# Kernel optimization log

Hardware: AMD Instinct MI355X
Metric: run time of the kernel (lower is better)

Reference implementation:

```python
import jax, jax.numpy as jnp
import numpy as np

NUM_CLASSES = 80
STRIDES = (8, 16, 32)


def _decode(p, stride):
    # p: [B, 5+C, H, W] raw head -> [B, HW, 5+C] decoded (xy in px, wh=exp*stride)
    B, C, H, W = p.shape
    ys, xs = jnp.meshgrid(jnp.arange(H), jnp.arange(W), indexing='ij')
    grid = jnp.stack([xs, ys], -1).reshape(H * W, 2).astype(p.dtype)
    out = p.reshape(B, C, H * W).transpose(0, 2, 1)
    xy = (out[..., :2] + grid) * stride
    wh = jnp.exp(out[..., 2:4]) * stride
    out = jnp.concatenate([xy, wh, out[..., 4:]], -1)
    es = jnp.full((H * W,), float(stride), p.dtype)
    return out, grid[:, 0], grid[:, 1], es


def _pairwise_iou(gt, pr):
    # gt [G,4] cxcywh, pr [A,4] -> [G,A]
    gt_tl = gt[:, None, :2] - gt[:, None, 2:] * 0.5
    gt_br = gt[:, None, :2] + gt[:, None, 2:] * 0.5
    pr_tl = pr[None, :, :2] - pr[None, :, 2:] * 0.5
    pr_br = pr[None, :, :2] + pr[None, :, 2:] * 0.5
    tl = jnp.maximum(gt_tl, pr_tl)
    br = jnp.minimum(gt_br, pr_br)
    en = jnp.all(tl < br, -1).astype(gt.dtype)
    inter = jnp.prod(br - tl, -1) * en
    a_gt = jnp.prod(gt[:, 2:], -1)[:, None]
    a_pr = jnp.prod(pr[:, 2:], -1)[None, :]
    return inter / (a_gt + a_pr - inter + 1e-16)


def _assign(gt_boxes, gt_cls, bbox, clsp, objp, xg, yg, es):
    # SimOTA assignment for one image (all fixed-shape; non-candidate anchors
    # are masked out via huge cost instead of boolean gather).
    G = gt_boxes.shape[0]
    xc = (xg + 0.5) * es  # [A] anchor centers
    yc = (yg + 0.5) * es
    gl = gt_boxes[:, 0:1] - 0.5 * gt_boxes[:, 2:3]
    gr = gt_boxes[:, 0:1] + 0.5 * gt_boxes[:, 2:3]
    gt_ = gt_boxes[:, 1:2] - 0.5 * gt_boxes[:, 3:4]
    gb = gt_boxes[:, 1:2] + 0.5 * gt_boxes[:, 3:4]
    in_box = (xc[None] > gl) & (xc[None] < gr) & (yc[None] > gt_) & (yc[None] < gb)  # [G,A]
    r = 2.5 * es[None]
    in_ctr = ((xc[None] > gt_boxes[:, 0:1] - r) & (xc[None] < gt_boxes[:, 0:1] + r)
              & (yc[None] > gt_boxes[:, 1:2] - r) & (yc[None] < gt_boxes[:, 1:2] + r))
    fg_cand = jnp.any(in_box, 0) | jnp.any(in_ctr, 0)  # [A]
    in_both = in_box & in_ctr  # [G,A]

    ious = _pairwise_iou(gt_boxes, bbox)  # [G,A]
    ious_m = jnp.where(fg_cand[None, :], ious, 0.0)
    iou_cost = -jnp.log(ious_m + 1e-8)

    # pairwise cls BCE cost: bce(sqrt(sigmoid(cls)*sigmoid(obj)), onehot(gt)).sum(-1)
    p = jnp.sqrt(jax.nn.sigmoid(clsp) * jax.nn.sigmoid(objp[:, None]))  # [A,C]
    lp = jnp.maximum(jnp.log(p), -100.0)
    l1p = jnp.maximum(jnp.log1p(-p), -100.0)
    t = jax.nn.one_hot(gt_cls, NUM_CLASSES, dtype=p.dtype)  # [G,C]
    cls_cost = -(jnp.einsum('ac,gc->ga', lp - l1p, t) + jnp.sum(l1p, -1)[None, :])

    cost = (cls_cost + 3.0 * iou_cost
            + 1e5 * (~in_both).astype(p.dtype)
            + 1e9 * (~fg_cand)[None, :].astype(p.dtype))

    # dynamic-k: k_g = clamp(sum(top10 ious), min=1)
    topk_ious, _ = jax.lax.top_k(ious_m, 10)
    dyn_k = jnp.clip(topk_ious.sum(-1).astype(jnp.int32), 1, None)  # [G]
    rank = jnp.argsort(jnp.argsort(cost, axis=1), axis=1)  # rank of each anchor per gt
    matching = (rank < dyn_k[:, None]) & fg_cand[None, :]  # [G,A]
    # resolve anchors matched to multiple gts: keep min-cost gt
    multi = matching.sum(0) > 1
    best = jnp.argmin(cost, 0)
    matching = jnp.where(multi[None, :], jnp.arange(G)[:, None] == best[None, :], matching)

    fg = jnp.any(matching, 0)  # [A]
    matched_gt = jnp.argmax(matching, 0)  # [A]
    pred_iou = jnp.sum(matching * ious, 0)  # [A]
    matched_cls = gt_cls[matched_gt]
    return fg, matched_gt, pred_iou, matched_cls


def _giou_loss(b, g):
    tl = jnp.maximum(b[..., :2] - b[..., 2:] * 0.5, g[..., :2] - g[..., 2:] * 0.5)
    br = jnp.minimum(b[..., :2] + b[..., 2:] * 0.5, g[..., :2] + g[..., 2:] * 0.5)
    area_b = jnp.prod(b[..., 2:], -1)
    area_g = jnp.prod(g[..., 2:], -1)
    en = jnp.all(tl < br, -1).astype(b.dtype)
    inter = jnp.prod(br - tl, -1) * en
    union = area_b + area_g - inter
    iou = inter / (union + 1e-16)
    ctl = jnp.minimum(b[..., :2] - b[..., 2:] * 0.5, g[..., :2] - g[..., 2:] * 0.5)
    cbr = jnp.maximum(b[..., :2] + b[..., 2:] * 0.5, g[..., :2] + g[..., 2:] * 0.5)
    area_c = jnp.maximum(jnp.prod(cbr - ctl, -1), 1e-16)
    giou = iou - (area_c - union) / area_c
    return 1.0 - jnp.clip(giou, -1.0, 1.0)


def _bce_logits(x, t):
    return jnp.maximum(x, 0.0) - x * t + jnp.log1p(jnp.exp(-jnp.abs(x)))


def _forward(p8, p16, p32, labels):
    outs, xo, yo, eo = [], [], [], []
    for p, s in zip((p8, p16, p32), STRIDES):
        o, x, y, e = _decode(p, s)
        outs.append(o); xo.append(x); yo.append(y); eo.append(e)
    outputs = jnp.concatenate(outs, 1)  # [B, A, 5+C]
    xg = jnp.concatenate(xo); yg = jnp.concatenate(yo); es = jnp.concatenate(eo)

    bbox = outputs[..., :4]
    obj = outputs[..., 4]
    cls = outputs[..., 5:]
    gt_boxes = labels[..., :4]
    gt_cls = labels[..., 4].astype(jnp.int32)

    # assignment runs under no_grad in torch
    det = jax.lax.stop_gradient(outputs)
    fg, matched_gt, pred_iou, matched_cls = jax.vmap(
        lambda gb, gc, o: _assign(gb, gc, o[..., :4], o[..., 5:], o[..., 4], xg, yg, es)
    )(gt_boxes, gt_cls, det)

    fgf = fg.astype(outputs.dtype)  # [B,A]
    reg_t = jnp.take_along_axis(gt_boxes, matched_gt[..., None], axis=1)  # [B,A,4]
    cls_t = (jax.nn.one_hot(matched_cls, NUM_CLASSES, dtype=outputs.dtype)
             * pred_iou[..., None] * fgf[..., None])

    loss_iou = jnp.sum(_giou_loss(bbox, reg_t) * fgf)
    loss_obj = jnp.sum(_bce_logits(obj, fgf))
    loss_cls = jnp.sum(_bce_logits(cls, cls_t) * fgf[..., None])
    num_fg = jnp.maximum(jnp.sum(fgf), 1.0)
    return (5.0 * loss_iou + loss_obj + loss_cls) / num_fg


def setup_inputs() -> dict:
    key = jax.random.key(0)
    k1, k2, k3, k4, k5, k6 = jax.random.split(key, 6)
    B, NGT = 32, 20
    p8 = jax.random.normal(k1, (B, 5 + NUM_CLASSES, 80, 80), dtype=jnp.float32)
    p16 = jax.random.normal(k2, (B, 5 + NUM_CLASSES, 40, 40), dtype=jnp.float32)
    p32 = jax.random.normal(k3, (B, 5 + NUM_CLASSES, 20, 20), dtype=jnp.float32)
    cxy = jax.random.uniform(k4, (B, NGT, 2), dtype=jnp.float32, minval=32.0, maxval=608.0)
    wh = jax.random.uniform(k5, (B, NGT, 2), dtype=jnp.float32, minval=16.0, maxval=128.0)
    cls = jax.random.randint(k6, (B, NGT, 1), 0, NUM_CLASSES).astype(jnp.float32)
    labels = jnp.concatenate([cxy, wh, cls], -1)
    return {"p8": p8, "p16": p16, "p32": p32, "labels": labels}


def reference(p8, p16, p32, labels):
    return _forward(p8, p16, p32, labels)
```

## Files before the change

### kernel.cpp

```cpp
#include <hip/hip_runtime.h>
#include <cstdint>
#include <cstddef>

#define NA 8400
#define NAP 8448
#define NB 32
#define NG 20
#define NCL 80
#define NBLK 33

__device__ __forceinline__ float frcp(float x) { return __builtin_amdgcn_rcpf(x); }
__device__ __forceinline__ float bce0(float x) {
  return fmaxf(x, 0.0f) + __logf(1.0f + __expf(-fabsf(x)));
}

__device__ __forceinline__ void anchor_info(int a, const float* p8, const float* p16,
                                            const float* p32, int b, const float*& base,
                                            int& hw, int& HW, int& xg, int& yg, float& fs) {
  if (a < 6400)      { hw = a;        HW = 6400; xg = hw % 80; yg = hw / 80; fs = 8.f;
                       base = p8  + (size_t)b * 85 * 6400; }
  else if (a < 8000) { hw = a - 6400; HW = 1600; xg = hw % 40; yg = hw / 40; fs = 16.f;
                       base = p16 + (size_t)b * 85 * 1600; }
  else               { hw = a - 8000; HW = 400;  xg = hw % 20; yg = hw / 20; fs = 32.f;
                       base = p32 + (size_t)b * 85 * 400; }
}

__device__ __forceinline__ float iou_raw(float gx, float gy, float gw, float gh, float4 p) {
  float gtlx = gx - gw * 0.5f, gtly = gy - gh * 0.5f;
  float gbrx = gx + gw * 0.5f, gbry = gy + gh * 0.5f;
  float ptlx = p.x - p.z * 0.5f, ptly = p.y - p.w * 0.5f;
  float pbrx = p.x + p.z * 0.5f, pbry = p.y + p.w * 0.5f;
  float tlx = fmaxf(gtlx, ptlx), tly = fmaxf(gtly, ptly);
  float brx = fminf(gbrx, pbrx), bry = fminf(gbry, pbry);
  float inter = ((tlx < brx) && (tly < bry)) ? (brx - tlx) * (bry - tly) : 0.0f;
  float ag = gw * gh, ap = p.z * p.w;
  return inter * frcp(ag + ap - inter + 1e-16f);
}

__device__ __forceinline__ float giou_loss(float4 bb, float gx, float gy, float gw, float gh) {
  float btlx = bb.x - bb.z * 0.5f, btly = bb.y - bb.w * 0.5f;
  float bbrx = bb.x + bb.z * 0.5f, bbry = bb.y + bb.w * 0.5f;
  float gtlx = gx - gw * 0.5f, gtly = gy - gh * 0.5f;
  float gbrx = gx + gw * 0.5f, gbry = gy + gh * 0.5f;
  float tlx = fmaxf(btlx, gtlx), tly = fmaxf(btly, gtly);
  float brx = fminf(bbrx, gbrx), bry = fminf(bbry, gbry);
  float area_b = bb.z * bb.w, area_g = gw * gh;
  float inter = ((tlx < brx) && (tly < bry)) ? (brx - tlx) * (bry - tly) : 0.0f;
  float uni = area_b + area_g - inter;
  float iou = inter / (uni + 1e-16f);
  float ctlx = fminf(btlx, gtlx), ctly = fminf(btly, gtly);
  float cbrx = fmaxf(bbrx, gbrx), cbry = fmaxf(bbry, gbry);
  float area_c = fmaxf((cbrx - ctlx) * (cbry - ctly), 1e-16f);
  float giou = iou - (area_c - uni) / area_c;
  giou = fminf(fmaxf(giou, -1.0f), 1.0f);
  return 1.0f - giou;
}

__device__ __forceinline__ void block_argmin(float& v, int& i, volatile float* s_v,
                                             volatile int* s_i, int tid) {
#pragma unroll
  for (int off = 32; off; off >>= 1) {
    float ov = __shfl_down(v, off, 64);
    int   oi = __shfl_down(i, off, 64);
    if (ov < v || (ov == v && oi < i)) { v = ov; i = oi; }
  }
  if ((tid & 63) == 0) { s_v[tid >> 6] = v; s_i[tid >> 6] = i; }
  __syncthreads();
  v = s_v[0]; i = s_i[0];
#pragma unroll
  for (int w = 1; w < 4; ++w) {
    float ov = s_v[w]; int oi = s_i[w];
    if (ov < v || (ov == v && oi < i)) { v = ov; i = oi; }
  }
}

__global__ __launch_bounds__(256) void k1(const float* __restrict__ p8,
                                          const float* __restrict__ p16,
                                          const float* __restrict__ p32,
                                          const float* __restrict__ labels,
                                          int* __restrict__ n_fg_cnt,
                                          int* __restrict__ fg_list,
                                          unsigned int* __restrict__ am_c,
                                          float4* __restrict__ bbox_c,
                                          float* __restrict__ lso_c,
                                          unsigned int* __restrict__ match_c,
                                          float* __restrict__ blk_obj) {
  __shared__ float s_gt[NG * 4];
  __shared__ unsigned int s_wcnt[4];
  __shared__ float s_part[4];
  __shared__ unsigned int s_base;
  int blk = blockIdx.x, b = blockIdx.y, tid = threadIdx.x, lane = tid & 63, wid = tid >> 6;

  if (tid < NG) {
    s_gt[tid * 4 + 0] = labels[((size_t)b * NG + tid) * 5 + 0];
    s_gt[tid * 4 + 1] = labels[((size_t)b * NG + tid) * 5 + 1];
    s_gt[tid * 4 + 2] = labels[((size_t)b * NG + tid) * 5 + 2];
    s_gt[tid * 4 + 3] = labels[((size_t)b * NG + tid) * 5 + 3];
  }
  __syncthreads();

  int a = blk * 256 + tid;
  match_c[(size_t)b * NAP + a] = 0u;

  bool fg = false;
  unsigned int msk = 0u;
  float bce_obj = 0.0f, obj = 0.0f;
  const float* base = nullptr; int hw = 0, HW = 0, xg = 0, yg = 0; float fs = 8.f;
  if (a < NA) {
    anchor_info(a, p8, p16, p32, b, base, hw, HW, xg, yg, fs);
    obj = base[4 * HW + hw];
    bce_obj = bce0(obj);
    float xc = ((float)xg + 0.5f) * fs;
    float yc = ((float)yg + 0.5f) * fs;
    float r = 2.5f * fs;
#pragma unroll
    for (int g = 0; g < NG; ++g) {
      float gx = s_gt[g * 4 + 0], gy = s_gt[g * 4 + 1];
      float gw = s_gt[g * 4 + 2], gh = s_gt[g * 4 + 3];
      bool inb = (xc > gx - 0.5f * gw) && (xc < gx + 0.5f * gw) &&
                 (yc > gy - 0.5f * gh) && (yc < gy + 0.5f * gh);
      bool inc = (xc > gx - r) && (xc < gx + r) && (yc > gy - r) && (yc < gy + r);
      fg = fg || inb || inc;
      if (inb && inc) msk |= (1u << g);
    }
  }

  unsigned long long bm = __ballot(fg);
#pragma unroll
  for (int off = 32; off; off >>= 1) bce_obj += __shfl_down(bce_obj, off, 64);
  if (lane == 0) { s_wcnt[wid] = (unsigned int)__popcll(bm); s_part[wid] = bce_obj; }
  __syncthreads();
  if (tid == 0) {
    unsigned int cnt = s_wcnt[0] + s_wcnt[1] + s_wcnt[2] + s_wcnt[3];
    s_base = cnt ? (unsigned int)atomicAdd(&n_fg_cnt[b], (int)cnt) : 0u;
    blk_obj[b * NBLK + blk] = s_part[0] + s_part[1] + s_part[2] + s_part[3];
  }
  __syncthreads();

  if (!fg) return;
  unsigned int pos = s_base;
  for (int w = 0; w < wid; ++w) pos += s_wcnt[w];
  pos += (unsigned int)__popcll(bm & ((1ull << lane) - 1ull));
  size_t bo = (size_t)b * NAP;
  int ci = (int)pos;
  fg_list[bo + ci] = a;
  am_c[bo + ci] = msk;

  float v0 = base[hw];
  float v1 = base[HW + hw];
  float v2 = base[2 * HW + hw];
  float v3 = base[3 * HW + hw];
  bbox_c[bo + ci] = make_float4((v0 + (float)xg) * fs, (v1 + (float)yg) * fs,
                                __expf(v2) * fs, __expf(v3) * fs);
  float uo = __logf(1.0f + __expf(-fabsf(obj)));
  lso_c[bo + ci] = fminf(obj, 0.0f) - uo;
}

__global__ __launch_bounds__(256) void k23(const float* __restrict__ p8,
                                           const float* __restrict__ p16,
                                           const float* __restrict__ p32,
                                           const float* __restrict__ labels,
                                           const int* __restrict__ fg_list,
                                           const int* __restrict__ n_fg,
                                           const float* __restrict__ lso_c,
                                           const unsigned int* __restrict__ am_c,
                                           const float4* __restrict__ bbox_c,
                                           float* __restrict__ sb_c,
                                           float* __restrict__ cost_tbl,
                                           float* __restrict__ iou_tbl) {
  __shared__ float s_gt[NG * 4];
  __shared__ int   s_gcls[NG];
  __shared__ float s_sl[8][33];
  __shared__ float s_sb[8][33];
  __shared__ float s_slr[32];
  int b = blockIdx.y, tid = threadIdx.x;
  int part = tid >> 5, cl = tid & 31;

  if (tid < NG) {
    s_gt[tid * 4 + 0] = labels[((size_t)b * NG + tid) * 5 + 0];
    s_gt[tid * 4 + 1] = labels[((size_t)b * NG + tid) * 5 + 1];
    s_gt[tid * 4 + 2] = labels[((size_t)b * NG + tid) * 5 + 2];
    s_gt[tid * 4 + 3] = labels[((size_t)b * NG + tid) * 5 + 3];
    s_gcls[tid] = (int)labels[((size_t)b * NG + tid) * 5 + 4];
  }
  __syncthreads();

  int n = n_fg[b];
  size_t bo = (size_t)b * NAP;

  for (int base_ci = blockIdx.x * 32; base_ci < n; base_ci += gridDim.x * 32) {
    int ci = base_ci + cl;
    bool act = ci < n;
    const float* base = nullptr; int hw = 0, HW = 0, xg, yg; float fs;
    float lso = 0.0f, sl = 0.0f, sb = 0.0f;
    if (act) {
      int a = fg_list[bo + ci];
      lso = lso_c[bo + ci];
      anchor_info(a, p8, p16, p32, b, base, hw, HW, xg, yg, fs);
      const float* cb = base + (size_t)(5 + part * 10) * HW + hw;
      float xs[10];
#pragma unroll
      for (int j = 0; j < 10; ++j) xs[j] = cb[(size_t)j * HW];
#pragma unroll
      for (int j = 0; j < 10; ++j) {
        float x = xs[j];
        float u = __logf(1.0f + __expf(-fabsf(x)));
        sb += fmaxf(x, 0.0f) + u;
        float lsx = fminf(x, 0.0f) - u;
        float lpr = 0.5f * (lsx + lso);
        float p   = __expf(lpr);
        sl += fmaxf(__logf(1.0f - p), -100.0f);
      }
    }
    s_sl[part][cl] = sl;
    s_sb[part][cl] = sb;
    __syncthreads();
    if (tid < 32) {
      float tsl = 0.0f, tsb = 0.0f;
#pragma unroll
      for (int q = 0; q < 8; ++q) { tsl += s_sl[q][tid]; tsb += s_sb[q][tid]; }
      s_slr[tid] = tsl;
      if (base_ci + tid < n) sb_c[bo + base_ci + tid] = tsb;
    }
    __syncthreads();
    if (act) {
      float slr = s_slr[cl];
      unsigned int am = am_c[bo + ci];
      float4 pb = bbox_c[bo + ci];
#pragma unroll
      for (int gg = 0; gg < 3; ++gg) {
        int g = part + (gg << 3);
        if (g < NG) {
          int cg = s_gcls[g];
          float x = base[(size_t)(5 + cg) * HW + hw];
          float u = __logf(1.0f + __expf(-fabsf(x)));
          float lsx = fminf(x, 0.0f) - u;
          float lpr = 0.5f * (lsx + lso);
          float p   = __expf(lpr);
          float l1p = fmaxf(__logf(1.0f - p), -100.0f);
          float wv  = fmaxf(lpr, -100.0f) - l1p;
          float iou = iou_raw(s_gt[g * 4 + 0], s_gt[g * 4 + 1],
                              s_gt[g * 4 + 2], s_gt[g * 4 + 3], pb);
          float cst = -(wv + slr) - 3.0f * __logf(iou + 1e-8f);
          if (!((am >> g) & 1u)) cst += 100000.0f;
          size_t row = ((size_t)b * NG + g) * NAP;
          cost_tbl[row + ci] = cst;
          iou_tbl[row + ci]  = iou;
        }
      }
    }
    __syncthreads();
  }
}

__global__ __launch_bounds__(256) void kBCD(const float* __restrict__ p8,
                                            const float* __restrict__ p16,
                                            const float* __restrict__ p32,
                                            const float* __restrict__ labels,
                                            const float* __restrict__ cost_tbl,
                                            const float* __restrict__ iou_tbl,
                                            const int* __restrict__ n_fg,
                                            unsigned int* __restrict__ match_c,
                                            const int* __restrict__ fg_list,
                                            const float4* __restrict__ bbox_c,
                                            const float* __restrict__ sb_c,
                                            const float* __restrict__ blk_obj,
                                            float* __restrict__ accum,
                                            int* __restrict__ done_g,
                                            int* __restrict__ done_img,
                                            float* __restrict__ out) {
  __shared__ float s_cost[NAP];
  __shared__ float s_wt[4 * 10];
  __shared__ float s_v[4];
  __shared__ int   s_i[4];
  __shared__ int   s_k;
  __shared__ int   s_flag;
  __shared__ float s_gt[NG * 5];
  __shared__ float s_red[16];

  int g = blockIdx.x, b = blockIdx.y, tid = threadIdx.x;
  int lane = tid & 63, wid = tid >> 6;
  int n = n_fg[b];
  size_t bo = (size_t)b * NAP;
  const float* __restrict__ cg = cost_tbl + ((size_t)b * NG + g) * NAP;
  const float* __restrict__ ig = iou_tbl  + ((size_t)b * NG + g) * NAP;

  float t10[10];
#pragma unroll
  for (int j = 0; j < 10; ++j) t10[j] = 0.0f;

  for (int ci = tid; ci < n; ci += 256) {
    float iou = ig[ci];
    float cst = cg[ci];
    if (iou > t10[9]) {
      t10[9] = iou;
#pragma unroll
      for (int q = 9; q > 0; --q) {
        if (t10[q] > t10[q - 1]) { float t = t10[q]; t10[q] = t10[q - 1]; t10[q - 1] = t; }
        else break;
      }
    }
    s_cost[ci] = cst;
  }

  for (int r = 0; r < 10; ++r) {
    float v = t10[0];
    float bv = v;
#pragma unroll
    for (int off = 32; off; off >>= 1) bv = fmaxf(bv, __shfl_down(bv, off, 64));
    bv = __shfl(bv, 0, 64);
    unsigned long long won = __ballot(v == bv);
    if (lane == __ffsll(won) - 1) {
#pragma unroll
      for (int q = 0; q < 9; ++q) t10[q] = t10[q + 1];
      t10[9] = -1.0f;
    }
    if (lane == 0) s_wt[wid * 10 + r] = bv;
  }
  __syncthreads();

  if (tid == 0) {
    int p0 = 0, p1 = 0, p2 = 0, p3 = 0;
    float s = 0.0f;
    for (int r = 0; r < 10; ++r) {
      float v0 = (p0 < 10) ? s_wt[p0]      : -2.0f;
      float v1 = (p1 < 10) ? s_wt[10 + p1] : -2.0f;
      float v2 = (p2 < 10) ? s_wt[20 + p2] : -2.0f;
      float v3 = (p3 < 10) ? s_wt[30 + p3] : -2.0f;
      float m = fmaxf(fmaxf(v0, v1), fmaxf(v2, v3));
      s += m;
      if (m == v0) ++p0; else if (m == v1) ++p1; else if (m == v2) ++p2; else ++p3;
    }
    int k = (int)s;
    if (k < 1) k = 1;
    s_k = k;
  }
  __syncthreads();
  int k = s_k;

  for (int it = 0; it < k; ++it) {
    float bv = 3.4e38f; int bi = NAP;
    for (int ci = tid; ci < n; ci += 256) {
      float v = s_cost[ci];
      if (v < bv || (v == bv && ci < bi)) { bv = v; bi = ci; }
    }
    block_argmin(bv, bi, s_v, s_i, tid);
    if (bv >= 1e8f) break;
    if (tid == 0) {
      atomicOr(&match_c[bo + bi], 1u << g);
      s_cost[bi] = 3.4e38f;
    }
    __syncthreads();
  }

  __syncthreads();
  if (tid == 0) {
    __threadfence();
    s_flag = (atomicAdd(&done_g[b], 1) == NG - 1) ? 1 : 0;
  }
  __syncthreads();
  if (!s_flag) return;

  if (tid < NG * 5) s_gt[tid] = labels[(size_t)b * NG * 5 + tid];
  __syncthreads();

  float li = 0.0f, oe = 0.0f, lc = 0.0f, nf = 0.0f;
  for (int ci = tid; ci < n; ci += 256) {
    unsigned int m = atomicOr(&match_c[bo + ci], 0u);
    if (m == 0u) continue;
    int mg;
    if (m & (m - 1)) {
      float bestc = 3.4e38f; mg = 0;
#pragma unroll 4
      for (int gq = 0; gq < NG; ++gq) {
        float cst = cost_tbl[((size_t)b * NG + gq) * NAP + ci];
        if (cst < bestc) { bestc = cst; mg = gq; }
      }
    } else {
      mg = __ffs(m) - 1;
    }
    int a = fg_list[bo + ci];
    const float* base; int hw, HW, xg, yg; float fs;
    anchor_info(a, p8, p16, p32, b, base, hw, HW, xg, yg, fs);
    float4 pb = bbox_c[bo + ci];
    float gx = s_gt[mg * 5], gy = s_gt[mg * 5 + 1];
    float gw = s_gt[mg * 5 + 2], gh = s_gt[mg * 5 + 3];
    int cgq = (int)s_gt[mg * 5 + 4];
    float piou = iou_tbl[((size_t)b * NG + mg) * NAP + ci];
    li += giou_loss(pb, gx, gy, gw, gh);
    float xcls = base[(size_t)(5 + cgq) * HW + hw];
    lc += sb_c[bo + ci] - xcls * piou;
    oe += base[4 * HW + hw];
    nf += 1.0f;
  }

  float vals[4] = {li, oe, lc, nf};
#pragma unroll
  for (int q = 0; q < 4; ++q) {
#pragma unroll
    for (int off = 32; off; off >>= 1) vals[q] += __shfl_down(vals[q], off, 64);
  }
  if ((tid & 63) == 0) {
    int w = tid >> 6;
    s_red[w * 4 + 0] = vals[0];
    s_red[w * 4 + 1] = vals[1];
    s_red[w * 4 + 2] = vals[2];
    s_red[w * 4 + 3] = vals[3];
  }
  __syncthreads();
  if (tid < 4) {
    const int slot[4] = {0, 2, 3, 4};
    float s = s_red[tid] + s_red[4 + tid] + s_red[8 + tid] + s_red[12 + tid];
    atomicAdd(&accum[slot[tid]], s);
  }

  if (tid == 0) {
    __threadfence();
    s_flag = (atomicAdd(done_img, 1) == NB - 1) ? 1 : 0;
  }
  __syncthreads();
  if (!s_flag) return;

  float s = 0.0f;
  for (int i = tid; i < NB * NBLK; i += 256) s += blk_obj[i];
#pragma unroll
  for (int off = 32; off; off >>= 1) s += __shfl_down(s, off, 64);
  if ((tid & 63) == 0) s_red[tid >> 6] = s;
  __syncthreads();
  if (tid == 0) {
    float obj_base = s_red[0] + s_red[1] + s_red[2] + s_red[3];
    float loss_iou = atomicAdd(&accum[0], 0.0f);
    float oex      = atomicAdd(&accum[2], 0.0f);
    float loss_cls = atomicAdd(&accum[3], 0.0f);
    float num_fg   = atomicAdd(&accum[4], 0.0f);
    float loss_obj = obj_base - oex;
    out[0] = (5.0f * loss_iou + loss_obj + loss_cls) / fmaxf(num_fg, 1.0f);
  }
}

extern "C" void kernel_launch(void* const* d_in, const int* in_sizes, int n_in,
                              void* d_out, int out_size, void* d_ws, size_t ws_size,
                              hipStream_t stream) {
  const float* p8     = (const float*)d_in[0];
  const float* p16    = (const float*)d_in[1];
  const float* p32    = (const float*)d_in[2];
  const float* labels = (const float*)d_in[3];
  float* out = (float*)d_out;

  const size_t BAP = (size_t)NB * NAP;
  char* w = (char*)d_ws;
  float4*       bbox_c   = (float4*)w;
  float*        cost_tbl = (float*)(w + BAP * 16);
  float*        iou_tbl  = cost_tbl + (size_t)NB * NG * NAP;
  char*         w2       = (char*)(iou_tbl + (size_t)NB * NG * NAP);
  int*          fg_list  = (int*)(w2);
  unsigned int* match_c  = (unsigned int*)(w2 + BAP * 4);
  float*        sb_c     = (float*)(w2 + BAP * 8);
  float*        lso_c    = (float*)(w2 + BAP * 12);
  unsigned int* am_c     = (unsigned int*)(w2 + BAP * 16);
  char*         w3       = w2 + BAP * 20;
  int*          n_fg     = (int*)w3;
  float*        accum    = (float*)(w3 + 128);
  int*          done_g   = (int*)(w3 + 256);
  int*          done_img = (int*)(w3 + 384);
  float*        blk_obj  = (float*)(w3 + 512);

  hipMemsetAsync(w3, 0, 512, stream);

  k1<<<dim3(NBLK, NB), dim3(256), 0, stream>>>(p8, p16, p32, labels, n_fg, fg_list, am_c,
                                               bbox_c, lso_c, match_c, blk_obj);
  k23<<<dim3(NBLK, NB), dim3(256), 0, stream>>>(p8, p16, p32, labels, fg_list, n_fg, lso_c,
                                                am_c, bbox_c, sb_c, cost_tbl, iou_tbl);
  kBCD<<<dim3(NG, NB), dim3(256), 0, stream>>>(p8, p16, p32, labels, cost_tbl, iou_tbl,
                                               n_fg, match_c, fg_list, bbox_c, sb_c,
                                               blk_obj, accum, done_g, done_img, out);
}
```

Before: 173.2 us.

## Fuse candidate compaction and cost kernels with per-block segmented compaction

Merges the candidate-filter kernel and the cost/IoU kernel into one kernel. Each block compacts its foreground anchors locally in shared memory, at fixed per-block offsets, instead of taking a global atomic slot. This removes one launch, the global atomic counter, and the global round trip for the lso, mask and bbox intermediates. In exchange, the assignment kernel must scan the full padded anchor range and use per-segment counts, which adds wasted iterations over empty slots in the argmin and loss loops.

```diff
diff --git a/kernel.cpp b/kernel.cpp
--- a/kernel.cpp
+++ b/kernel.cpp
@@ -74,33 +74,47 @@
   }
 }
 
-__global__ __launch_bounds__(256) void k1(const float* __restrict__ p8,
+__global__ __launch_bounds__(256) void kF(const float* __restrict__ p8,
                                           const float* __restrict__ p16,
                                           const float* __restrict__ p32,
                                           const float* __restrict__ labels,
-                                          int* __restrict__ n_fg_cnt,
-                                          int* __restrict__ fg_list,
-                                          unsigned int* __restrict__ am_c,
+                                          int* __restrict__ n_seg,
+                                          int* __restrict__ a_seg,
                                           float4* __restrict__ bbox_c,
-                                          float* __restrict__ lso_c,
+                                          float* __restrict__ sb_c,
+                                          float* __restrict__ cost_tbl,
+                                          float* __restrict__ iou_tbl,
                                           unsigned int* __restrict__ match_c,
                                           float* __restrict__ blk_obj) {
   __shared__ float s_gt[NG * 4];
+  __shared__ int   s_gcls[NG];
+  __shared__ int   s_a[256];
+  __shared__ unsigned int s_msk[256];
+  __shared__ float s_lso[256];
+  __shared__ float4 s_bb[256];
   __shared__ unsigned int s_wcnt[4];
   __shared__ float s_part[4];
-  __shared__ unsigned int s_base;
+  __shared__ int   s_cnt;
+  __shared__ float s_sl[8][33];
+  __shared__ float s_sb[8][33];
+  __shared__ float s_slr[32];
+
   int blk = blockIdx.x, b = blockIdx.y, tid = threadIdx.x, lane = tid & 63, wid = tid >> 6;
+  int part = tid >> 5, cl = tid & 31;
 
   if (tid < NG) {
     s_gt[tid * 4 + 0] = labels[((size_t)b * NG + tid) * 5 + 0];
     s_gt[tid * 4 + 1] = labels[((size_t)b * NG + tid) * 5 + 1];
     s_gt[tid * 4 + 2] = labels[((size_t)b * NG + tid) * 5 + 2];
     s_gt[tid * 4 + 3] = labels[((size_t)b * NG + tid) * 5 + 3];
-  }
-  __syncthreads();
-
-  int a = blk * 256 + tid;
-  match_c[(size_t)b * NAP + a] = 0u;
+    s_gcls[tid] = (int)labels[((size_t)b * NG + tid) * 5 + 4];
+  }
+  __syncthreads();
+
+  size_t bo = (size_t)b * NAP;
+  int ci0 = blk * 256;
+  int a = ci0 + tid;
+  match_c[bo + a] = 0u;
 
   bool fg = false;
   unsigned int msk = 0u;
@@ -131,76 +145,45 @@
   if (lane == 0) { s_wcnt[wid] = (unsigned int)__popcll(bm); s_part[wid] = bce_obj; }
   __syncthreads();
   if (tid == 0) {
-    unsigned int cnt = s_wcnt[0] + s_wcnt[1] + s_wcnt[2] + s_wcnt[3];
-    s_base = cnt ? (unsigned int)atomicAdd(&n_fg_cnt[b], (int)cnt) : 0u;
+    int cnt = (int)(s_wcnt[0] + s_wcnt[1] + s_wcnt[2] + s_wcnt[3]);
+    s_cnt = cnt;
+    n_seg[b * NBLK + blk] = cnt;
     blk_obj[b * NBLK + blk] = s_part[0] + s_part[1] + s_part[2] + s_part[3];
   }
-  __syncthreads();
-
-  if (!fg) return;
-  unsigned int pos = s_base;
-  for (int w = 0; w < wid; ++w) pos += s_wcnt[w];
-  pos += (unsigned int)__popcll(bm & ((1ull << lane) - 1ull));
-  size_t bo = (size_t)b * NAP;
-  int ci = (int)pos;
-  fg_list[bo + ci] = a;
-  am_c[bo + ci] = msk;
-
-  float v0 = base[hw];
-  float v1 = base[HW + hw];
-  float v2 = base[2 * HW + hw];
-  float v3 = base[3 * HW + hw];
-  bbox_c[bo + ci] = make_float4((v0 + (float)xg) * fs, (v1 + (float)yg) * fs,
-                                __expf(v2) * fs, __expf(v3) * fs);
-  float uo = __logf(1.0f + __expf(-fabsf(obj)));
-  lso_c[bo + ci] = fminf(obj, 0.0f) - uo;
-}
-
-__global__ __launch_bounds__(256) void k23(const float* __restrict__ p8,
-                                           const float* __restrict__ p16,
-                                           const float* __restrict__ p32,
-                                           const float* __restrict__ labels,
-                                           const int* __restrict__ fg_list,
-                                           const int* __restrict__ n_fg,
-                                           const float* __restrict__ lso_c,
-                                           const unsigned int* __restrict__ am_c,
-                                           const float4* __restrict__ bbox_c,
-                                           float* __restrict__ sb_c,
-                                           float* __restrict__ cost_tbl,
-                                           float* __restrict__ iou_tbl) {
-  __shared__ float s_gt[NG * 4];
-  __shared__ int   s_gcls[NG];
-  __shared__ float s_sl[8][33];
-  __shared__ float s_sb[8][33];
-  __shared__ float s_slr[32];
-  int b = blockIdx.y, tid = threadIdx.x;
-  int part = tid >> 5, cl = tid & 31;
-
-  if (tid < NG) {
-    s_gt[tid * 4 + 0] = labels[((size_t)b * NG + tid) * 5 + 0];
-    s_gt[tid * 4 + 1] = labels[((size_t)b * NG + tid) * 5 + 1];
-    s_gt[tid * 4 + 2] = labels[((size_t)b * NG + tid) * 5 + 2];
-    s_gt[tid * 4 + 3] = labels[((size_t)b * NG + tid) * 5 + 3];
-    s_gcls[tid] = (int)labels[((size_t)b * NG + tid) * 5 + 4];
-  }
-  __syncthreads();
-
-  int n = n_fg[b];
-  size_t bo = (size_t)b * NAP;
-
-  for (int base_ci = blockIdx.x * 32; base_ci < n; base_ci += gridDim.x * 32) {
-    int ci = base_ci + cl;
-    bool act = ci < n;
-    const float* base = nullptr; int hw = 0, HW = 0, xg, yg; float fs;
+  if (fg) {
+    unsigned int li = 0;
+    for (int w = 0; w < wid; ++w) li += s_wcnt[w];
+    li += (unsigned int)__popcll(bm & ((1ull << lane) - 1ull));
+    s_a[li] = a;
+    s_msk[li] = msk;
+    float v0 = base[hw];
+    float v1 = base[HW + hw];
+    float v2 = base[2 * HW + hw];
+    float v3 = base[3 * HW + hw];
+    float4 pb = make_float4((v0 + (float)xg) * fs, (v1 + (float)yg) * fs,
+                            __expf(v2) * fs, __expf(v3) * fs);
+    s_bb[li] = pb;
+    float uo = __logf(1.0f + __expf(-fabsf(obj)));
+    s_lso[li] = fminf(obj, 0.0f) - uo;
+    a_seg[bo + ci0 + li] = a;
+    bbox_c[bo + ci0 + li] = pb;
+  }
+  __syncthreads();
+
+  int cnt = s_cnt;
+  for (int t0 = 0; t0 < cnt; t0 += 32) {
+    int idx = t0 + cl;
+    bool act = idx < cnt;
+    const float* cbase = nullptr; int chw = 0, cHW = 0, cxg, cyg; float cfs;
     float lso = 0.0f, sl = 0.0f, sb = 0.0f;
     if (act) {
-      int a = fg_list[bo + ci];
-      lso = lso_c[bo + ci];
-      anchor_info(a, p8, p16, p32, b, base, hw, HW, xg, yg, fs);
-      const float* cb = base + (size_t)(5 + part * 10) * HW + hw;
+      int aa = s_a[idx];
+      lso = s_lso[idx];
+      anchor_info(aa, p8, p16, p32, b, cbase, chw, cHW, cxg, cyg, cfs);
+      const float* cb = cbase + (size_t)(5 + part * 10) * cHW + chw;
       float xs[10];
 #pragma unroll
-      for (int j = 0; j < 10; ++j) xs[j] = cb[(size_t)j * HW];
+      for (int j = 0; j < 10; ++j) xs[j] = cb[(size_t)j * cHW];
 #pragma unroll
       for (int j = 0; j < 10; ++j) {
         float x = xs[j];
@@ -220,19 +203,19 @@
 #pragma unroll
       for (int q = 0; q < 8; ++q) { tsl += s_sl[q][tid]; tsb += s_sb[q][tid]; }
       s_slr[tid] = tsl;
-      if (base_ci + tid < n) sb_c[bo + base_ci + tid] = tsb;
+      if (t0 + tid < cnt) sb_c[bo + ci0 + t0 + tid] = tsb;
     }
     __syncthreads();
     if (act) {
       float slr = s_slr[cl];
-      unsigned int am = am_c[bo + ci];
-      float4 pb = bbox_c[bo + ci];
+      unsigned int am = s_msk[idx];
+      float4 pb = s_bb[idx];
 #pragma unroll
       for (int gg = 0; gg < 3; ++gg) {
         int g = part + (gg << 3);
         if (g < NG) {
           int cg = s_gcls[g];
-          float x = base[(size_t)(5 + cg) * HW + hw];
+          float x = cbase[(size_t)(5 + cg) * cHW + chw];
           float u = __logf(1.0f + __expf(-fabsf(x)));
           float lsx = fminf(x, 0.0f) - u;
           float lpr = 0.5f * (lsx + lso);
@@ -244,8 +227,8 @@
           float cst = -(wv + slr) - 3.0f * __logf(iou + 1e-8f);
           if (!((am >> g) & 1u)) cst += 100000.0f;
           size_t row = ((size_t)b * NG + g) * NAP;
-          cost_tbl[row + ci] = cst;
-          iou_tbl[row + ci]  = iou;
+          cost_tbl[row + ci0 + idx] = cst;
+          iou_tbl[row + ci0 + idx]  = iou;
         }
       }
     }
@@ -259,9 +242,9 @@
                                             const float* __restrict__ labels,
                                             const float* __restrict__ cost_tbl,
                                             const float* __restrict__ iou_tbl,
-                                            const int* __restrict__ n_fg,
+                                            const int* __restrict__ n_seg,
                                             unsigned int* __restrict__ match_c,
-                                            const int* __restrict__ fg_list,
+                                            const int* __restrict__ a_seg,
                                             const float4* __restrict__ bbox_c,
                                             const float* __restrict__ sb_c,
                                             const float* __restrict__ blk_obj,
@@ -270,6 +253,7 @@
                                             int* __restrict__ done_img,
                                             float* __restrict__ out) {
   __shared__ float s_cost[NAP];
+  __shared__ int   s_nseg[NBLK];
   __shared__ float s_wt[4 * 10];
   __shared__ float s_v[4];
   __shared__ int   s_i[4];
@@ -280,18 +264,22 @@
 
   int g = blockIdx.x, b = blockIdx.y, tid = threadIdx.x;
   int lane = tid & 63, wid = tid >> 6;
-  int n = n_fg[b];
   size_t bo = (size_t)b * NAP;
   const float* __restrict__ cg = cost_tbl + ((size_t)b * NG + g) * NAP;
   const float* __restrict__ ig = iou_tbl  + ((size_t)b * NG + g) * NAP;
 
+  if (tid < NBLK) s_nseg[tid] = n_seg[b * NBLK + tid];
+  __syncthreads();
+
   float t10[10];
 #pragma unroll
   for (int j = 0; j < 10; ++j) t10[j] = 0.0f;
 
-  for (int ci = tid; ci < n; ci += 256) {
-    float iou = ig[ci];
-    float cst = cg[ci];
+  for (int it = 0; it < NBLK; ++it) {
+    int ci = it * 256 + tid;
+    bool valid = tid < s_nseg[it];
+    float iou = valid ? ig[ci] : 0.0f;
+    float cst = valid ? cg[ci] : 1e9f;
     if (iou > t10[9]) {
       t10[9] = iou;
 #pragma unroll
@@ -340,7 +328,7 @@
 
   for (int it = 0; it < k; ++it) {
     float bv = 3.4e38f; int bi = NAP;
-    for (int ci = tid; ci < n; ci += 256) {
+    for (int ci = tid; ci < NAP; ci += 256) {
       float v = s_cost[ci];
       if (v < bv || (v == bv && ci < bi)) { bv = v; bi = ci; }
     }
@@ -365,7 +353,7 @@
   __syncthreads();
 
   float li = 0.0f, oe = 0.0f, lc = 0.0f, nf = 0.0f;
-  for (int ci = tid; ci < n; ci += 256) {
+  for (int ci = tid; ci < NAP; ci += 256) {
     unsigned int m = atomicOr(&match_c[bo + ci], 0u);
     if (m == 0u) continue;
     int mg;
@@ -379,7 +367,7 @@
     } else {
       mg = __ffs(m) - 1;
     }
-    int a = fg_list[bo + ci];
+    int a = a_seg[bo + ci];
     const float* base; int hw, HW, xg, yg; float fs;
     anchor_info(a, p8, p16, p32, b, base, hw, HW, xg, yg, fs);
     float4 pb = bbox_c[bo + ci];
@@ -453,25 +441,22 @@
   float*        cost_tbl = (float*)(w + BAP * 16);
   float*        iou_tbl  = cost_tbl + (size_t)NB * NG * NAP;
   char*         w2       = (char*)(iou_tbl + (size_t)NB * NG * NAP);
-  int*          fg_list  = (int*)(w2);
+  int*          a_seg    = (int*)(w2);
   unsigned int* match_c  = (unsigned int*)(w2 + BAP * 4);
   float*        sb_c     = (float*)(w2 + BAP * 8);
-  float*        lso_c    = (float*)(w2 + BAP * 12);
-  unsigned int* am_c     = (unsigned int*)(w2 + BAP * 16);
-  char*         w3       = w2 + BAP * 20;
-  int*          n_fg     = (int*)w3;
-  float*        accum    = (float*)(w3 + 128);
-  int*          done_g   = (int*)(w3 + 256);
-  int*          done_img = (int*)(w3 + 384);
-  float*        blk_obj  = (float*)(w3 + 512);
+  char*         w3       = w2 + BAP * 12;
+  float*        accum    = (float*)(w3);
+  int*          done_g   = (int*)(w3 + 128);
+  int*          done_img = (int*)(w3 + 256);
+  int*          n_seg    = (int*)(w3 + 512);
+  float*        blk_obj  = (float*)(w3 + 512 + NB * NBLK * 4);
 
   hipMemsetAsync(w3, 0, 512, stream);
 
-  k1<<<dim3(NBLK, NB), dim3(256), 0, stream>>>(p8, p16, p32, labels, n_fg, fg_list, am_c,
-                                               bbox_c, lso_c, match_c, blk_obj);
-  k23<<<dim3(NBLK, NB), dim3(256), 0, stream>>>(p8, p16, p32, labels, fg_list, n_fg, lso_c,
-                                                am_c, bbox_c, sb_c, cost_tbl, iou_tbl);
+  kF<<<dim3(NBLK, NB), dim3(256), 0, stream>>>(p8, p16, p32, labels, n_seg, a_seg,
+                                               bbox_c, sb_c, cost_tbl, iou_tbl,
+                                               match_c, blk_obj);
   kBCD<<<dim3(NG, NB), dim3(256), 0, stream>>>(p8, p16, p32, labels, cost_tbl, iou_tbl,
-                                               n_fg, match_c, fg_list, bbox_c, sb_c,
+                                               n_seg, match_c, a_seg, bbox_c, sb_c,
                                                blk_obj, accum, done_g, done_img, out);
 }
```

Result: slower. 194.5 us (+12.3%).
